# Performance work log

Measured on AMD Instinct MI355X. Metric: run time of the kernel, lower is better.

Reference implementation:

```python
import jax, jax.numpy as jnp
import numpy as np

B, S, D = 2, 4096, 512
H, DK, DV = 8, 64, 64
LN_EPS = 1e-5
ATTN_EPS = 1e-6


def layer_norm(x, g, b):
    mu = jnp.mean(x, axis=-1, keepdims=True)
    var = jnp.var(x, axis=-1, keepdims=True)
    return (x - mu) * jax.lax.rsqrt(var + LN_EPS) * g + b


def setup_inputs() -> dict:
    key = jax.random.key(0)
    ks = jax.random.split(key, 12)
    s = 1.0 / np.sqrt(D)
    inp = {
        "Q": jax.random.normal(ks[0], (B, S, D), jnp.float32),
        "K": jax.random.normal(ks[1], (B, S, D), jnp.float32),
        "V": jax.random.normal(ks[2], (B, S, D), jnp.float32),
        "W_q": jax.random.normal(ks[3], (D, H * DK), jnp.float32) * s,
        "W_k": jax.random.normal(ks[4], (D, H * DK), jnp.float32) * s,
        "W_v": jax.random.normal(ks[5], (D, H * DV), jnp.float32) * s,
        "W_o": jax.random.normal(ks[6], (H * DV, D), jnp.float32) * s,
        "ln1_g": jnp.ones((D,), jnp.float32),
        "ln1_b": jnp.zeros((D,), jnp.float32),
        "ln2_g": jnp.ones((D,), jnp.float32),
        "ln2_b": jnp.zeros((D,), jnp.float32),
        "w1": jax.random.normal(ks[7], (4 * D, D), jnp.float32) * s,  # torch Linear: (out, in)
        "b1": jnp.zeros((4 * D,), jnp.float32),
        "w2": jax.random.normal(ks[8], (D, 4 * D), jnp.float32) * (1.0 / np.sqrt(4 * D)),
        "b2": jnp.zeros((D,), jnp.float32),
    }
    return inp


def reference(Q, K, V, W_q, W_k, W_v, W_o, ln1_g, ln1_b, ln2_g, ln2_b, w1, b1, w2, b2):
    Qn = layer_norm(Q, ln1_g, ln1_b)
    # project and split heads: [B,S,H,dk] -> [B,H,S,dk]
    q = (Qn @ W_q).reshape(B, S, H, DK).transpose(0, 2, 1, 3)
    k = (K @ W_k).reshape(B, S, H, DK).transpose(0, 2, 1, 3)
    v = (V @ W_v).reshape(B, S, H, DV).transpose(0, 2, 1, 3)
    scores = jnp.einsum("bhqd,bhkd->bhqk", q, k) / (np.sqrt(DK) + ATTN_EPS)
    attn = jax.nn.softmax(scores, axis=-1)  # same as max-subtract softmax
    ctx = jnp.einsum("bhqk,bhkd->bhqd", attn, v)
    ctx = ctx.transpose(0, 2, 1, 3).reshape(B, S, H * DV)
    att_out = ctx @ W_o  # dropout = identity (eval)
    X = Q + att_out
    Xn = layer_norm(X, ln2_g, ln2_b)
    h = jax.nn.gelu(Xn @ w1.T + b1, approximate=False)
    ffn = h @ w2.T + b2
    return X + ffn
```

## Files before the change

kernel.cpp:

```cpp
#include <hip/hip_runtime.h>

typedef unsigned short u16;
typedef __attribute__((ext_vector_type(8))) short short8;
typedef __attribute__((ext_vector_type(4))) float f32x4;

struct __align__(8) us4 { u16 x, y, z, w; };
struct __align__(8) ui2 { unsigned x, y; };

#define CEXP (1.44269504089f / (8.0f + 1e-6f))

__device__ __forceinline__ u16 f2bf(float f) {
  unsigned u = __builtin_bit_cast(unsigned, f);
  unsigned r = (u + 0x7FFFu + ((u >> 16) & 1u)) >> 16;
  return (u16)r;
}

__device__ __forceinline__ unsigned pack_bf2_trunc(float a, float b) {
  return __builtin_amdgcn_perm(__builtin_bit_cast(unsigned, b),
                               __builtin_bit_cast(unsigned, a), 0x07060302u);
}

__device__ __forceinline__ void async_load16(const void* g, void* l) {
  __builtin_amdgcn_global_load_lds((const __attribute__((address_space(1))) void*)g,
                                   (__attribute__((address_space(3))) void*)l, 16, 0, 0);
}

__global__ void prep_weights(const float* __restrict__ Wq, const float* __restrict__ Wk,
                             const float* __restrict__ Wv, const float* __restrict__ Wo,
                             const float* __restrict__ w1, const float* __restrict__ w2,
                             u16* __restrict__ wqkvT, u16* __restrict__ woT,
                             u16* __restrict__ w1b, u16* __restrict__ w2b) {
  const int z = blockIdx.y;
  const int stride = gridDim.x * blockDim.x;
  const int i0 = blockIdx.x * blockDim.x + threadIdx.x;
  if (z < 4) {
    const float* src = z == 0 ? Wq : z == 1 ? Wk : z == 2 ? Wv : Wo;
    u16* dst = z < 3 ? wqkvT + z * 512 * 512 : woT;
    const float scale = (z == 0) ? CEXP : 1.0f;
    for (int i = i0; i < 512 * 512; i += stride) {
      int k = i >> 9, n = i & 511;
      dst[(size_t)n * 512 + k] = f2bf(src[i] * scale);
    }
  } else {
    const float* src = z == 4 ? w1 : w2;
    u16* dst = z == 4 ? w1b : w2b;
    for (int i = i0; i < 2048 * 512; i += stride) dst[i] = f2bf(src[i]);
  }
}

template <bool KV>
__launch_bounds__(128)
__global__ void ln_cast(const float* __restrict__ X, const float* __restrict__ gw,
                        const float* __restrict__ bw, u16* __restrict__ Y,
                        const float* __restrict__ Kin, const float* __restrict__ Vin,
                        u16* __restrict__ Kb, u16* __restrict__ Vb) {
  const int row = blockIdx.x, t = threadIdx.x;
  const size_t base = (size_t)row * 512;
  float4 x = ((const float4*)(X + base))[t];
  float s = x.x + x.y + x.z + x.w;
  float ss = x.x * x.x + x.y * x.y + x.z * x.z + x.w * x.w;
#pragma unroll
  for (int off = 32; off > 0; off >>= 1) {
    s += __shfl_xor(s, off);
    ss += __shfl_xor(ss, off);
  }
  __shared__ float red[4];
  if ((t & 63) == 0) { red[(t >> 6) * 2] = s; red[(t >> 6) * 2 + 1] = ss; }
  __syncthreads();
  const float tot = red[0] + red[2], tss = red[1] + red[3];
  const float mu = tot * (1.0f / 512.0f);
  const float var = tss * (1.0f / 512.0f) - mu * mu;
  const float rs = rsqrtf(var + 1e-5f);
  float4 g4 = ((const float4*)gw)[t];
  float4 b4 = ((const float4*)bw)[t];
  us4 o;
  o.x = f2bf((x.x - mu) * rs * g4.x + b4.x);
  o.y = f2bf((x.y - mu) * rs * g4.y + b4.y);
  o.z = f2bf((x.z - mu) * rs * g4.z + b4.z);
  o.w = f2bf((x.w - mu) * rs * g4.w + b4.w);
  ((us4*)(Y + base))[t] = o;
  if constexpr (KV) {
    float4 k4 = ((const float4*)(Kin + base))[t];
    float4 v4 = ((const float4*)(Vin + base))[t];
    us4 ko, vo;
    ko.x = f2bf(k4.x); ko.y = f2bf(k4.y); ko.z = f2bf(k4.z); ko.w = f2bf(k4.w);
    vo.x = f2bf(v4.x); vo.y = f2bf(v4.y); vo.z = f2bf(v4.z); vo.w = f2bf(v4.w);
    ((us4*)(Kb + base))[t] = ko;
    ((us4*)(Vb + base))[t] = vo;
  }
}

__launch_bounds__(256, 3)
__global__ void gemm_qkv(const u16* __restrict__ Aq, const u16* __restrict__ Ak,
                         const u16* __restrict__ Av, const u16* __restrict__ Bt,
                         u16* __restrict__ qb, u16* __restrict__ kb, u16* __restrict__ vtb) {
  __shared__ __align__(16) u16 sA[128 * 32];
  __shared__ __align__(16) u16 sB[128 * 32];
  const int tid = threadIdx.x;
  const int wave = tid >> 6, lane = tid & 63;
  const int l15 = lane & 15, quad = lane >> 4;
  const int qsw = (quad ^ ((l15 >> 1) & 3)) * 8;
  const int m0 = blockIdx.x * 128, n0 = blockIdx.y * 128;
  const int sel = n0 >> 9;
  const u16* A = sel == 0 ? Aq : sel == 1 ? Ak : Av;
  const int wm = (wave >> 1) * 64, wn = (wave & 1) * 64;
  const int u0 = wave * 64 + lane, u1 = u0 + 256;
  const int sw0 = ((u0 & 3) ^ ((u0 >> 3) & 3)) * 8;
  const int K = 512;

  const u16* a0 = A + (size_t)(m0 + (u0 >> 2)) * K + sw0;
  const u16* a1 = A + (size_t)(m0 + (u1 >> 2)) * K + sw0;
  const u16* b0 = Bt + (size_t)(n0 + (u0 >> 2)) * K + sw0;
  const u16* b1p = Bt + (size_t)(n0 + (u1 >> 2)) * K + sw0;

  f32x4 acc[4][4] = {};
  for (int k0 = 0; k0 < K; k0 += 32) {
    async_load16(a0 + k0, &sA[wave * 512]);
    async_load16(a1 + k0, &sA[2048 + wave * 512]);
    async_load16(b0 + k0, &sB[wave * 512]);
    async_load16(b1p + k0, &sB[2048 + wave * 512]);
    __syncthreads();
    short8 af[4], bfr[4];
#pragma unroll
    for (int i = 0; i < 4; i++)
      af[i] = *(const short8*)&sA[(wm + i * 16 + l15) * 32 + qsw];
#pragma unroll
    for (int j = 0; j < 4; j++)
      bfr[j] = *(const short8*)&sB[(wn + j * 16 + l15) * 32 + qsw];
#pragma unroll
    for (int i = 0; i < 4; i++)
#pragma unroll
      for (int j = 0; j < 4; j++)
        acc[i][j] = __builtin_amdgcn_mfma_f32_16x16x32_bf16(af[i], bfr[j], acc[i][j], 0, 0, 0);
    __syncthreads();
  }

#pragma unroll
  for (int i = 0; i < 4; i++) {
#pragma unroll
    for (int j = 0; j < 4; j++) {
      const int ocol = ((n0 + wn) & 511) + j * 16 + l15;
      const int row0 = m0 + wm + i * 16 + quad * 4;
      if (sel < 2) {
        u16* C = sel == 0 ? qb : kb;
#pragma unroll
        for (int r = 0; r < 4; r++) C[(size_t)(row0 + r) * 512 + ocol] = f2bf(acc[i][j][r]);
      } else {
        const int b = row0 >> 12, s0 = row0 & 4095;
        const int hh = ocol >> 6, cc = ocol & 63;
        us4 pk;
        pk.x = f2bf(acc[i][j][0]); pk.y = f2bf(acc[i][j][1]);
        pk.z = f2bf(acc[i][j][2]); pk.w = f2bf(acc[i][j][3]);
        *(us4*)&vtb[((size_t)((b * 8 + hh) * 64 + cc) << 12) + s0] = pk;
      }
    }
  }
}

template <int EP, int TN, int LB>
__launch_bounds__(256, LB)
__global__ void gemm_bt(const u16* __restrict__ A, const u16* __restrict__ Bt,
                        int M, int N, int K, void* __restrict__ Cp,
                        const float* __restrict__ bias, const float* __restrict__ res) {
  constexpr int MI = (TN == 128) ? 4 : 2;
  __shared__ __align__(16) u16 sA[128 * 32];
  __shared__ __align__(16) u16 sB[TN * 32];
  const int tid = threadIdx.x;
  const int wave = tid >> 6, lane = tid & 63;
  const int l15 = lane & 15, quad = lane >> 4;
  const int qsw = (quad ^ ((l15 >> 1) & 3)) * 8;
  const int m0 = blockIdx.x * 128, n0 = blockIdx.y * TN;
  const int wm = (TN == 128) ? (wave >> 1) * 64 : wave * 32;
  const int wn = (TN == 128) ? (wave & 1) * 64 : 0;
  const int u0 = wave * 64 + lane, u1 = u0 + 256;
  const int sw0 = ((u0 & 3) ^ ((u0 >> 3) & 3)) * 8;

  const u16* a0 = A + (size_t)(m0 + (u0 >> 2)) * K + sw0;
  const u16* a1 = A + (size_t)(m0 + (u1 >> 2)) * K + sw0;
  const u16* b0 = Bt + (size_t)(n0 + (u0 >> 2)) * K + sw0;

  f32x4 acc[MI][4] = {};
  for (int k0 = 0; k0 < K; k0 += 32) {
    async_load16(a0 + k0, &sA[wave * 512]);
    async_load16(a1 + k0, &sA[2048 + wave * 512]);
    async_load16(b0 + k0, &sB[wave * 512]);
    if constexpr (TN == 128) {
      const u16* b1p = Bt + (size_t)(n0 + (u1 >> 2)) * K + sw0;
      async_load16(b1p + k0, &sB[2048 + wave * 512]);
    }
    __syncthreads();
    short8 af[MI], bfr[4];
#pragma unroll
    for (int i = 0; i < MI; i++)
      af[i] = *(const short8*)&sA[(wm + i * 16 + l15) * 32 + qsw];
#pragma unroll
    for (int j = 0; j < 4; j++)
      bfr[j] = *(const short8*)&sB[(wn + j * 16 + l15) * 32 + qsw];
#pragma unroll
    for (int i = 0; i < MI; i++)
#pragma unroll
      for (int j = 0; j < 4; j++)
        acc[i][j] = __builtin_amdgcn_mfma_f32_16x16x32_bf16(af[i], bfr[j], acc[i][j], 0, 0, 0);
    __syncthreads();
  }

#pragma unroll
  for (int i = 0; i < MI; i++) {
#pragma unroll
    for (int j = 0; j < 4; j++) {
      const int col = n0 + wn + j * 16 + l15;
      const int row0 = m0 + wm + i * 16 + quad * 4;
      if (EP == 2) {
        float* C = (float*)Cp;
#pragma unroll
        for (int r = 0; r < 4; r++) {
          size_t idx = (size_t)(row0 + r) * N + col;
          C[idx] = acc[i][j][r] + res[idx];
        }
      } else if (EP == 3) {
        u16* C = (u16*)Cp;
        const float bv = bias[col];
#pragma unroll
        for (int r = 0; r < 4; r++) {
          float xx = acc[i][j][r] + bv;
          float gl = 0.5f * xx * (1.0f + erff(xx * 0.70710678118f));
          C[(size_t)(row0 + r) * N + col] = f2bf(gl);
        }
      } else {
        float* C = (float*)Cp;
        const float bv = bias[col];
#pragma unroll
        for (int r = 0; r < 4; r++) {
          size_t idx = (size_t)(row0 + r) * N + col;
          C[idx] = acc[i][j][r] + bv + res[idx];
        }
      }
    }
  }
}

__launch_bounds__(256, 3)
__global__ void attn_kernel(const u16* __restrict__ qb, const u16* __restrict__ kb,
                            const u16* __restrict__ vtb, float* __restrict__ po,
                            float* __restrict__ pl) {
  __shared__ __align__(16) u16 sK[2 * 128 * 32];
  __shared__ __align__(16) u16 sV[4 * 64 * 32];
  __shared__ __align__(16) u16 sP[4 * 32 * 40];
  const int tid = threadIdx.x;
  const int wave = tid >> 6, lane = tid & 63;
  const int l15 = lane & 15, quad = lane >> 4;
  const int qsw = (quad ^ ((l15 >> 1) & 3)) * 8;
  const int bh = blockIdx.y, b = bh >> 3, h = bh & 7;
  const int q0 = blockIdx.x * 128;
  const int ks = blockIdx.z;
  const size_t rb = (size_t)b * 4096;

  short8 qf[2][2];
#pragma unroll
  for (int mi = 0; mi < 2; mi++)
#pragma unroll
    for (int kk = 0; kk < 2; kk++) {
      int row = q0 + wave * 32 + mi * 16 + l15;
      qf[mi][kk] = *(const short8*)&qb[(rb + row) * 512 + h * 64 + kk * 32 + quad * 8];
    }

  f32x4 o_t[2][4] = {};
  float l_part[2] = {0.f, 0.f};
  u16* myP = &sP[wave * 32 * 40];

  for (int jt = 0; jt < 16; jt++) {
    const int j0 = ks * 2048 + jt * 128;
#pragma unroll
    for (int r = 0; r < 4; r++) {
      int u = r * 256 + wave * 64 + lane;
      int kk = u >> 9, key = (u >> 2) & 127, c8 = (u & 3) ^ ((u >> 3) & 3);
      async_load16(&kb[(rb + j0 + key) * 512 + h * 64 + kk * 32 + c8 * 8],
                   &sK[(r * 256 + wave * 64) * 8]);
    }
#pragma unroll
    for (int r = 0; r < 4; r++) {
      int u = r * 256 + wave * 64 + lane;
      int kk = u >> 8, vc = (u >> 2) & 63, c8 = (u & 3) ^ ((u >> 3) & 3);
      async_load16(&vtb[((size_t)(bh * 64 + vc)) * 4096 + j0 + kk * 32 + c8 * 8],
                   &sV[(r * 256 + wave * 64) * 8]);
    }
    __syncthreads();

#pragma unroll
    for (int kk = 0; kk < 4; kk++) {
#pragma unroll
      for (int nh = 0; nh < 2; nh++) {
        const int ni = kk * 2 + nh;
        short8 af0 = *(const short8*)&sK[(ni * 16 + l15) * 32 + qsw];
        short8 af1 = *(const short8*)&sK[4096 + (ni * 16 + l15) * 32 + qsw];
#pragma unroll
        for (int mi = 0; mi < 2; mi++) {
          f32x4 st = {};
          st = __builtin_amdgcn_mfma_f32_16x16x32_bf16(af0, qf[mi][0], st, 0, 0, 0);
          st = __builtin_amdgcn_mfma_f32_16x16x32_bf16(af1, qf[mi][1], st, 0, 0, 0);
          float p0 = __builtin_amdgcn_exp2f(st[0]);
          float p1 = __builtin_amdgcn_exp2f(st[1]);
          float p2 = __builtin_amdgcn_exp2f(st[2]);
          float p3 = __builtin_amdgcn_exp2f(st[3]);
          l_part[mi] += (p0 + p1) + (p2 + p3);
          ui2 wv;
          wv.x = pack_bf2_trunc(p0, p1);
          wv.y = pack_bf2_trunc(p2, p3);
          *(ui2*)&myP[(mi * 16 + l15) * 40 + nh * 16 + quad * 4] = wv;
        }
      }
      asm volatile("s_waitcnt lgkmcnt(0)" ::: "memory");
      short8 pf[2], vf[4];
#pragma unroll
      for (int mi = 0; mi < 2; mi++)
        pf[mi] = *(const short8*)&myP[(mi * 16 + l15) * 40 + quad * 8];
#pragma unroll
      for (int vi = 0; vi < 4; vi++)
        vf[vi] = *(const short8*)&sV[kk * 2048 + (vi * 16 + l15) * 32 + qsw];
#pragma unroll
      for (int mi = 0; mi < 2; mi++)
#pragma unroll
        for (int vi = 0; vi < 4; vi++)
          o_t[mi][vi] = __builtin_amdgcn_mfma_f32_16x16x32_bf16(vf[vi], pf[mi], o_t[mi][vi], 0, 0, 0);
    }
    __syncthreads();
  }

#pragma unroll
  for (int mi = 0; mi < 2; mi++) {
    float l = l_part[mi];
    l += __shfl_xor(l, 16);
    l += __shfl_xor(l, 32);
    const int qrow = q0 + wave * 32 + mi * 16 + l15;
    if (quad == 0) pl[(size_t)ks * 65536 + (rb + qrow) * 8 + h] = l;
#pragma unroll
    for (int vi = 0; vi < 4; vi++)
      *(f32x4*)&po[(size_t)ks * 4194304 + (rb + qrow) * 512 + h * 64 + vi * 16 + quad * 4] =
          o_t[mi][vi];
  }
}

__launch_bounds__(128)
__global__ void attn_merge(const float* __restrict__ po, const float* __restrict__ pl,
                           u16* __restrict__ ctx) {
  const int row = blockIdx.x, t = threadIdx.x;
  const int col = t * 4, h = col >> 6;
  const size_t idx = (size_t)row * 512 + col;
  const float l = pl[row * 8 + h] + pl[65536 + row * 8 + h];
  f32x4 a = *(const f32x4*)&po[idx];
  f32x4 c = *(const f32x4*)&po[4194304 + idx];
  const float inv = 1.0f / l;
  us4 o;
  o.x = f2bf((a[0] + c[0]) * inv);
  o.y = f2bf((a[1] + c[1]) * inv);
  o.z = f2bf((a[2] + c[2]) * inv);
  o.w = f2bf((a[3] + c[3]) * inv);
  *(us4*)&ctx[idx] = o;
}

extern "C" void kernel_launch(void* const* d_in, const int* in_sizes, int n_in,
                              void* d_out, int out_size, void* d_ws, size_t ws_size,
                              hipStream_t stream) {
  (void)in_sizes; (void)n_in; (void)out_size; (void)ws_size;
  const float* Q = (const float*)d_in[0];
  const float* K = (const float*)d_in[1];
  const float* V = (const float*)d_in[2];
  const float* W_q = (const float*)d_in[3];
  const float* W_k = (const float*)d_in[4];
  const float* W_v = (const float*)d_in[5];
  const float* W_o = (const float*)d_in[6];
  const float* ln1_g = (const float*)d_in[7];
  const float* ln1_b = (const float*)d_in[8];
  const float* ln2_g = (const float*)d_in[9];
  const float* ln2_b = (const float*)d_in[10];
  const float* w1 = (const float*)d_in[11];
  const float* b1 = (const float*)d_in[12];
  const float* w2 = (const float*)d_in[13];
  const float* b2 = (const float*)d_in[14];

  char* w = (char*)d_ws;
  const size_t MB = 1u << 20;
  u16* wqkvT = (u16*)(w);
  u16* woT = (u16*)(w + 3 * MB / 2);
  u16* w1b = (u16*)(w + 2 * MB);
  u16* w2b = (u16*)(w + 4 * MB);
  u16* Qn  = (u16*)(w + 6 * MB);
  u16* Kb  = (u16*)(w + 14 * MB);
  u16* Vb  = (u16*)(w + 22 * MB);
  u16* qb  = (u16*)(w + 30 * MB);
  u16* kb  = (u16*)(w + 38 * MB);
  u16* vtb = (u16*)(w + 46 * MB);
  u16* ctx = (u16*)(w + 54 * MB);
  float* X = (float*)(w + 94 * MB);
  float* po = (float*)(w + 62 * MB);
  float* pl = (float*)(w + 6 * MB);
  u16* Xn  = (u16*)(w + 6 * MB + MB);
  Xn = (u16*)(w + 6 * MB);
  u16* hb  = (u16*)(w + 14 * MB);

  prep_weights<<<dim3(128, 6), 256, 0, stream>>>(W_q, W_k, W_v, W_o, w1, w2,
                                                 wqkvT, woT, w1b, w2b);
  ln_cast<true><<<8192, 128, 0, stream>>>(Q, ln1_g, ln1_b, Qn, K, V, Kb, Vb);
  gemm_qkv<<<dim3(64, 12), 256, 0, stream>>>(Qn, Kb, Vb, wqkvT, qb, kb, vtb);
  attn_kernel<<<dim3(32, 16, 2), 256, 0, stream>>>(qb, kb, vtb, po, pl);
  attn_merge<<<8192, 128, 0, stream>>>(po, pl, ctx);
  gemm_bt<2, 64, 3><<<dim3(64, 8), 256, 0, stream>>>(ctx, woT, 8192, 512, 512, X, nullptr, Q);
  ln_cast<false><<<8192, 128, 0, stream>>>(X, ln2_g, ln2_b, Xn, nullptr, nullptr, nullptr, nullptr);
  gemm_bt<3, 128, 3><<<dim3(64, 16), 256, 0, stream>>>(Xn, w1b, 8192, 2048, 512, hb, b1, nullptr);
  gemm_bt<4, 64, 3><<<dim3(64, 8), 256, 0, stream>>>(hb, w2b, 8192, 512, 2048, (float*)d_out, b2, X);
}
```

Before: 351.4 us.

## Enlarge attention query tiles, split keys four ways, store bf16 partials, tile weight transpose

```diff
diff --git a/kernel.cpp b/kernel.cpp
--- a/kernel.cpp
+++ b/kernel.cpp
@@ -13,6 +13,9 @@
   unsigned u = __builtin_bit_cast(unsigned, f);
   unsigned r = (u + 0x7FFFu + ((u >> 16) & 1u)) >> 16;
   return (u16)r;
+}
+__device__ __forceinline__ float bf2f(u16 v) {
+  return __builtin_bit_cast(float, (unsigned)v << 16);
 }
 
 __device__ __forceinline__ unsigned pack_bf2_trunc(float a, float b) {
@@ -31,20 +34,42 @@
                              u16* __restrict__ wqkvT, u16* __restrict__ woT,
                              u16* __restrict__ w1b, u16* __restrict__ w2b) {
   const int z = blockIdx.y;
-  const int stride = gridDim.x * blockDim.x;
-  const int i0 = blockIdx.x * blockDim.x + threadIdx.x;
+  const int t = threadIdx.x;
   if (z < 4) {
     const float* src = z == 0 ? Wq : z == 1 ? Wk : z == 2 ? Wv : Wo;
     u16* dst = z < 3 ? wqkvT + z * 512 * 512 : woT;
     const float scale = (z == 0) ? CEXP : 1.0f;
-    for (int i = i0; i < 512 * 512; i += stride) {
-      int k = i >> 9, n = i & 511;
-      dst[(size_t)n * 512 + k] = f2bf(src[i] * scale);
+    __shared__ float tl[64][65];
+    const int ti = blockIdx.x >> 3, tj = blockIdx.x & 7;
+    const int tx = t & 15, ty = t >> 4;
+#pragma unroll
+    for (int rr = 0; rr < 4; rr++) {
+      const int row = rr * 16 + ty;
+      float4 v = *(const float4*)&src[(size_t)(ti * 64 + row) * 512 + tj * 64 + tx * 4];
+      tl[row][tx * 4 + 0] = v.x; tl[row][tx * 4 + 1] = v.y;
+      tl[row][tx * 4 + 2] = v.z; tl[row][tx * 4 + 3] = v.w;
+    }
+    __syncthreads();
+#pragma unroll
+    for (int rr = 0; rr < 4; rr++) {
+      const int row = rr * 16 + ty;
+      us4 o;
+      o.x = f2bf(tl[tx * 4 + 0][row] * scale);
+      o.y = f2bf(tl[tx * 4 + 1][row] * scale);
+      o.z = f2bf(tl[tx * 4 + 2][row] * scale);
+      o.w = f2bf(tl[tx * 4 + 3][row] * scale);
+      *(us4*)&dst[(size_t)(tj * 64 + row) * 512 + ti * 64 + tx * 4] = o;
     }
   } else {
     const float* src = z == 4 ? w1 : w2;
     u16* dst = z == 4 ? w1b : w2b;
-    for (int i = i0; i < 2048 * 512; i += stride) dst[i] = f2bf(src[i]);
+    const int stride = gridDim.x * blockDim.x;
+    for (int i = blockIdx.x * blockDim.x + t; i < 2048 * 512 / 4; i += stride) {
+      float4 v = ((const float4*)src)[i];
+      us4 o;
+      o.x = f2bf(v.x); o.y = f2bf(v.y); o.z = f2bf(v.z); o.w = f2bf(v.w);
+      ((us4*)dst)[i] = o;
+    }
   }
 }
 
@@ -241,35 +266,35 @@
 
 __launch_bounds__(256, 3)
 __global__ void attn_kernel(const u16* __restrict__ qb, const u16* __restrict__ kb,
-                            const u16* __restrict__ vtb, float* __restrict__ po,
+                            const u16* __restrict__ vtb, u16* __restrict__ po,
                             float* __restrict__ pl) {
   __shared__ __align__(16) u16 sK[2 * 128 * 32];
   __shared__ __align__(16) u16 sV[4 * 64 * 32];
-  __shared__ __align__(16) u16 sP[4 * 32 * 40];
+  __shared__ __align__(16) u16 sP[4 * 64 * 40];
   const int tid = threadIdx.x;
   const int wave = tid >> 6, lane = tid & 63;
   const int l15 = lane & 15, quad = lane >> 4;
   const int qsw = (quad ^ ((l15 >> 1) & 3)) * 8;
   const int bh = blockIdx.y, b = bh >> 3, h = bh & 7;
-  const int q0 = blockIdx.x * 128;
+  const int q0 = blockIdx.x * 256;
   const int ks = blockIdx.z;
   const size_t rb = (size_t)b * 4096;
 
-  short8 qf[2][2];
-#pragma unroll
-  for (int mi = 0; mi < 2; mi++)
+  short8 qf[4][2];
+#pragma unroll
+  for (int mi = 0; mi < 4; mi++)
 #pragma unroll
     for (int kk = 0; kk < 2; kk++) {
-      int row = q0 + wave * 32 + mi * 16 + l15;
+      int row = q0 + wave * 64 + mi * 16 + l15;
       qf[mi][kk] = *(const short8*)&qb[(rb + row) * 512 + h * 64 + kk * 32 + quad * 8];
     }
 
-  f32x4 o_t[2][4] = {};
-  float l_part[2] = {0.f, 0.f};
-  u16* myP = &sP[wave * 32 * 40];
-
-  for (int jt = 0; jt < 16; jt++) {
-    const int j0 = ks * 2048 + jt * 128;
+  f32x4 o_t[4][4] = {};
+  float l_part[4] = {0.f, 0.f, 0.f, 0.f};
+  u16* myP = &sP[wave * 64 * 40];
+
+  for (int jt = 0; jt < 8; jt++) {
+    const int j0 = ks * 1024 + jt * 128;
 #pragma unroll
     for (int r = 0; r < 4; r++) {
       int u = r * 256 + wave * 64 + lane;
@@ -294,7 +319,7 @@
         short8 af0 = *(const short8*)&sK[(ni * 16 + l15) * 32 + qsw];
         short8 af1 = *(const short8*)&sK[4096 + (ni * 16 + l15) * 32 + qsw];
 #pragma unroll
-        for (int mi = 0; mi < 2; mi++) {
+        for (int mi = 0; mi < 4; mi++) {
           f32x4 st = {};
           st = __builtin_amdgcn_mfma_f32_16x16x32_bf16(af0, qf[mi][0], st, 0, 0, 0);
           st = __builtin_amdgcn_mfma_f32_16x16x32_bf16(af1, qf[mi][1], st, 0, 0, 0);
@@ -310,15 +335,15 @@
         }
       }
       asm volatile("s_waitcnt lgkmcnt(0)" ::: "memory");
-      short8 pf[2], vf[4];
-#pragma unroll
-      for (int mi = 0; mi < 2; mi++)
+      short8 pf[4], vf[4];
+#pragma unroll
+      for (int mi = 0; mi < 4; mi++)
         pf[mi] = *(const short8*)&myP[(mi * 16 + l15) * 40 + quad * 8];
 #pragma unroll
       for (int vi = 0; vi < 4; vi++)
         vf[vi] = *(const short8*)&sV[kk * 2048 + (vi * 16 + l15) * 32 + qsw];
 #pragma unroll
-      for (int mi = 0; mi < 2; mi++)
+      for (int mi = 0; mi < 4; mi++)
 #pragma unroll
         for (int vi = 0; vi < 4; vi++)
           o_t[mi][vi] = __builtin_amdgcn_mfma_f32_16x16x32_bf16(vf[vi], pf[mi], o_t[mi][vi], 0, 0, 0);
@@ -327,34 +352,41 @@
   }
 
 #pragma unroll
-  for (int mi = 0; mi < 2; mi++) {
+  for (int mi = 0; mi < 4; mi++) {
     float l = l_part[mi];
     l += __shfl_xor(l, 16);
     l += __shfl_xor(l, 32);
-    const int qrow = q0 + wave * 32 + mi * 16 + l15;
+    const int qrow = q0 + wave * 64 + mi * 16 + l15;
     if (quad == 0) pl[(size_t)ks * 65536 + (rb + qrow) * 8 + h] = l;
 #pragma unroll
-    for (int vi = 0; vi < 4; vi++)
-      *(f32x4*)&po[(size_t)ks * 4194304 + (rb + qrow) * 512 + h * 64 + vi * 16 + quad * 4] =
-          o_t[mi][vi];
+    for (int vi = 0; vi < 4; vi++) {
+      us4 o;
+      o.x = f2bf(o_t[mi][vi][0]); o.y = f2bf(o_t[mi][vi][1]);
+      o.z = f2bf(o_t[mi][vi][2]); o.w = f2bf(o_t[mi][vi][3]);
+      *(us4*)&po[(size_t)ks * 4194304 + (rb + qrow) * 512 + h * 64 + vi * 16 + quad * 4] = o;
+    }
   }
 }
 
 __launch_bounds__(128)
-__global__ void attn_merge(const float* __restrict__ po, const float* __restrict__ pl,
+__global__ void attn_merge(const u16* __restrict__ po, const float* __restrict__ pl,
                            u16* __restrict__ ctx) {
   const int row = blockIdx.x, t = threadIdx.x;
   const int col = t * 4, h = col >> 6;
   const size_t idx = (size_t)row * 512 + col;
-  const float l = pl[row * 8 + h] + pl[65536 + row * 8 + h];
-  f32x4 a = *(const f32x4*)&po[idx];
-  f32x4 c = *(const f32x4*)&po[4194304 + idx];
+  float l = 0.f;
+#pragma unroll
+  for (int ks = 0; ks < 4; ks++) l += pl[(size_t)ks * 65536 + row * 8 + h];
+  float o0 = 0.f, o1 = 0.f, o2 = 0.f, o3 = 0.f;
+#pragma unroll
+  for (int ks = 0; ks < 4; ks++) {
+    us4 v = *(const us4*)&po[(size_t)ks * 4194304 + idx];
+    o0 += bf2f(v.x); o1 += bf2f(v.y); o2 += bf2f(v.z); o3 += bf2f(v.w);
+  }
   const float inv = 1.0f / l;
   us4 o;
-  o.x = f2bf((a[0] + c[0]) * inv);
-  o.y = f2bf((a[1] + c[1]) * inv);
-  o.z = f2bf((a[2] + c[2]) * inv);
-  o.w = f2bf((a[3] + c[3]) * inv);
+  o.x = f2bf(o0 * inv); o.y = f2bf(o1 * inv);
+  o.z = f2bf(o2 * inv); o.w = f2bf(o3 * inv);
   *(us4*)&ctx[idx] = o;
 }
 
@@ -391,18 +423,17 @@
   u16* kb  = (u16*)(w + 38 * MB);
   u16* vtb = (u16*)(w + 46 * MB);
   u16* ctx = (u16*)(w + 54 * MB);
+  u16* po  = (u16*)(w + 62 * MB);
+  float* pl = (float*)(w + 6 * MB);
   float* X = (float*)(w + 94 * MB);
-  float* po = (float*)(w + 62 * MB);
-  float* pl = (float*)(w + 6 * MB);
-  u16* Xn  = (u16*)(w + 6 * MB + MB);
-  Xn = (u16*)(w + 6 * MB);
+  u16* Xn  = (u16*)(w + 6 * MB);
   u16* hb  = (u16*)(w + 14 * MB);
 
-  prep_weights<<<dim3(128, 6), 256, 0, stream>>>(W_q, W_k, W_v, W_o, w1, w2,
-                                                 wqkvT, woT, w1b, w2b);
+  prep_weights<<<dim3(64, 6), 256, 0, stream>>>(W_q, W_k, W_v, W_o, w1, w2,
+                                                wqkvT, woT, w1b, w2b);
   ln_cast<true><<<8192, 128, 0, stream>>>(Q, ln1_g, ln1_b, Qn, K, V, Kb, Vb);
   gemm_qkv<<<dim3(64, 12), 256, 0, stream>>>(Qn, Kb, Vb, wqkvT, qb, kb, vtb);
-  attn_kernel<<<dim3(32, 16, 2), 256, 0, stream>>>(qb, kb, vtb, po, pl);
+  attn_kernel<<<dim3(16, 16, 4), 256, 0, stream>>>(qb, kb, vtb, po, pl);
   attn_merge<<<8192, 128, 0, stream>>>(po, pl, ctx);
   gemm_bt<2, 64, 3><<<dim3(64, 8), 256, 0, stream>>>(ctx, woT, 8192, 512, 512, X, nullptr, Q);
   ln_cast<false><<<8192, 128, 0, stream>>>(X, ln2_g, ln2_b, Xn, nullptr, nullptr, nullptr, nullptr);
```

Result: slower. 412.6 us (+17.4%).
